# Kernel tuning notes

Hardware: AMD Instinct MI355X
Metric: run time of the kernel (lower is better)

The kernel has to match this reference:

```python
import jax, jax.numpy as jnp
from jax import lax
import numpy as np

B, T, C, V, E, H, OC = 1024, 32, 14, 21128, 200, 50, 8


def gru(x, Wih, Whh, bih, bhh):
    # x: [N, T, E] -> hiddens [N, T, H]; torch nn.GRU gate order (r, z, n)
    Hd = Whh.shape[1]
    xp = jnp.einsum('nte,ge->ntg', x, Wih) + bih  # [N, T, 3H]
    h0 = jnp.zeros((x.shape[0], Hd), x.dtype)

    def step(h, xt):
        gh = h @ Whh.T + bhh
        r = jax.nn.sigmoid(xt[:, :Hd] + gh[:, :Hd])
        z = jax.nn.sigmoid(xt[:, Hd:2 * Hd] + gh[:, Hd:2 * Hd])
        n = jnp.tanh(xt[:, 2 * Hd:] + r * gh[:, 2 * Hd:])
        h_new = (1.0 - z) * n + z * h
        return h_new, h_new

    _, hs = lax.scan(step, h0, jnp.swapaxes(xp, 0, 1))
    return jnp.swapaxes(hs, 0, 1)


def setup_inputs():
    key = jax.random.key(0)
    ks = jax.random.split(key, 32)
    s = 0.1
    inp = {
        'contexts_indices': jax.random.randint(ks[0], (B, T), 0, V),
        'candidates_indices': jax.random.randint(ks[1], (B, C, T), 0, V),
        'y_dev': jax.random.uniform(ks[2], (B, C), dtype=jnp.float32),
        'emb': jax.random.normal(ks[3], (V, E), dtype=jnp.float32),
        'A': jax.random.normal(ks[4], (H, H), dtype=jnp.float32) * s,
        'Wih_c': jax.random.normal(ks[5], (3 * H, E), dtype=jnp.float32) * s,
        'Whh_c': jax.random.normal(ks[6], (3 * H, H), dtype=jnp.float32) * s,
        'bih_c': jnp.zeros((3 * H,), jnp.float32),
        'bhh_c': jnp.zeros((3 * H,), jnp.float32),
        'Wih_r': jax.random.normal(ks[7], (3 * H, E), dtype=jnp.float32) * s,
        'Whh_r': jax.random.normal(ks[8], (3 * H, H), dtype=jnp.float32) * s,
        'bih_r': jnp.zeros((3 * H,), jnp.float32),
        'bhh_r': jnp.zeros((3 * H,), jnp.float32),
        'conv_w': jax.random.normal(ks[9], (OC, 2, 3, 3), dtype=jnp.float32) * s,
        'Wih2': jax.random.normal(ks[10], (3 * H, OC * 10 * 10), dtype=jnp.float32) * s,
        'Whh2': jax.random.normal(ks[11], (3 * H, H), dtype=jnp.float32) * s,
        'bih2': jnp.zeros((3 * H,), jnp.float32),
        'bhh2': jnp.zeros((3 * H,), jnp.float32),
        'fc1_w': jax.random.normal(ks[12], (100, C * H), dtype=jnp.float32) * s,
        'fc1_b': jnp.zeros((100,), jnp.float32),
        'fc2_w': jax.random.normal(ks[13], (C, 100), dtype=jnp.float32) * s,
        'fc2_b': jnp.zeros((C,), jnp.float32),
    }
    return inp


def reference(contexts_indices, candidates_indices, y_dev, emb, A,
              Wih_c, Whh_c, bih_c, bhh_c, Wih_r, Whh_r, bih_r, bhh_r,
              conv_w, Wih2, Whh2, bih2, bhh2, fc1_w, fc1_b, fc2_w, fc2_b):
    b = contexts_indices.shape[0]
    ctx = contexts_indices[:, None, :]                      # [B,1,T]
    ctx_emb = emb[ctx]                                      # [B,1,T,E] (dropout = identity in eval)
    cand_emb = emb[candidates_indices]                      # [B,C,T,E]

    ctx_h = gru(ctx_emb.reshape(-1, T, E), Wih_c, Whh_c, bih_c, bhh_c).reshape(b, 1, T, H)
    cand_h = gru(cand_emb.reshape(-1, T, E), Wih_r, Whh_r, bih_r, bhh_r).reshape(b, C, T, H)

    M1 = jnp.einsum('btph,bcqh->btcpq', ctx_emb, cand_emb)  # [B,1,C,T,T]
    ctx_hA = jnp.einsum('btij,jk->btik', ctx_h, A)
    M2 = jnp.einsum('btph,bcqh->btcpq', ctx_hA, cand_h)

    # faithful to torch: stack on dim 2 then row-major view(-1, 2, T, T)
    M = jnp.stack([M1, M2], axis=2).reshape(-1, 2, T, T)    # [B*C, 2, T, T]

    conv = lax.conv_general_dilated(M, conv_w, (1, 1), 'VALID',
                                    dimension_numbers=('NCHW', 'OIHW', 'NCHW'))  # [B*C, OC, 30, 30]
    pooled = lax.reduce_window(conv, -jnp.inf, lax.max,
                               (1, 1, 3, 3), (1, 1, 3, 3), 'VALID')              # [B*C, OC, 10, 10]

    feats = pooled.reshape(b, C, OC * 10 * 10)              # [B, C, 800]
    Hs = gru(feats, Wih2, Whh2, bih2, bhh2)                 # [B, C, H]
    flat = Hs.reshape(b, -1)                                # [B, C*H]

    hid = jax.nn.relu(flat @ fc1_w.T + fc1_b)
    log_probs = jax.nn.log_softmax(hid @ fc2_w.T + fc2_b, axis=-1)  # softmax then log
    kl = jnp.where(y_dev > 0, y_dev * (jnp.log(y_dev) - log_probs), 0.0)
    return jnp.mean(kl)
```

## Files before the change

kernel.cpp:

```cpp
#include <hip/hip_runtime.h>
#include <math.h>

typedef unsigned short u16;
typedef short s16;
typedef u16 u16x8 __attribute__((ext_vector_type(8)));
typedef s16 short8v __attribute__((ext_vector_type(8)));
typedef float f32x4 __attribute__((ext_vector_type(4)));

__device__ __forceinline__ float b2f(u16 u) {
    return __uint_as_float(((unsigned)u) << 16);
}
__device__ __forceinline__ u16 f2b(float f) {
    unsigned u = __float_as_uint(f);
    unsigned r = (u + 0x7FFFu + ((u >> 16) & 1u)) >> 16;
    return (u16)r;
}

__global__ __launch_bounds__(256) void k_cvt_all(
    const float* __restrict__ emb, u16* __restrict__ embh,
    const float* __restrict__ wcf, u16* __restrict__ wch,
    const float* __restrict__ wrf, u16* __restrict__ wrh,
    const float* __restrict__ w2f, u16* __restrict__ w2h)
{
    long j = (long)blockIdx.x * 256 + threadIdx.x;
    if (j < 1056400) {
        float4 v = ((const float4*)emb)[j];
        *(ushort4*)(embh + j * 4) = make_ushort4(f2b(v.x), f2b(v.y), f2b(v.z), f2b(v.w));
        return;
    }
    j -= 1056400;
    if (j < 7500) {
        float4 v = ((const float4*)wcf)[j];
        *(ushort4*)(wch + j * 4) = make_ushort4(f2b(v.x), f2b(v.y), f2b(v.z), f2b(v.w));
        return;
    }
    j -= 7500;
    if (j < 7500) {
        float4 v = ((const float4*)wrf)[j];
        *(ushort4*)(wrh + j * 4) = make_ushort4(f2b(v.x), f2b(v.y), f2b(v.z), f2b(v.w));
        return;
    }
    j -= 7500;
    if (j < 120000) {
        int jj = (int)(j / 800), k = (int)(j % 800);
        int p = k >> 3, oc = k & 7;
        w2h[jj * 800 + k] = f2b(w2f[jj * 800 + oc * 100 + p]);
    }
}

__global__ __launch_bounds__(256) void k_projmm2(
    const u16* __restrict__ embh, const u16* __restrict__ wc,
    const u16* __restrict__ wr, const float* __restrict__ bc,
    const float* __restrict__ br, u16* __restrict__ outc,
    u16* __restrict__ outr, int V)
{
    __shared__ s16 Ab[2048];
    __shared__ s16 Bb[2560];
    __shared__ float bhL[160];
    const int t = threadIdx.x;
    const int w = t >> 6, l = t & 63, lg = l >> 4, lr = l & 15;
    int id = blockIdx.x;
    const int half = (id >= 662) ? 1 : 0;
    id -= half * 662;
    const u16* wh = half ? wr : wc;
    const float* bias = half ? br : bc;
    u16* outp = half ? outr : outc;
    const int mb = id >> 1, nb = id & 1;
    const long rowbase = (long)mb * 64;
    const int colbase = nb * 80;
    if (t < 160) bhL[t] = (t < 150) ? bias[t] : 0.f;

    f32x4 acc[5];
#pragma unroll
    for (int i = 0; i < 5; ++i) acc[i] = (f32x4){0,0,0,0};

    for (int ch = 0; ch < 7; ++ch) {
        __syncthreads();
        {
            int kc = t >> 6, row = t & 63;
            long grow = rowbase + row; if (grow >= V) grow = V - 1;
            int k0 = ch * 32 + kc * 8;
            short8v v = {0,0,0,0,0,0,0,0};
            if (k0 < 200) v = *(const short8v*)(embh + grow * 200 + k0);
            *(short8v*)&Ab[t * 8] = v;
        }
        for (int it = t; it < 320; it += 256) {
            int kc = it / 80, col = it % 80;
            int gcol = colbase + col;
            int k0 = ch * 32 + kc * 8;
            short8v v = {0,0,0,0,0,0,0,0};
            if (gcol < 150 && k0 < 200)
                v = *(const short8v*)(wh + (size_t)gcol * 200 + k0);
            *(short8v*)&Bb[it * 8] = v;
        }
        __syncthreads();
        short8v a = *(short8v*)&Ab[(lg * 64 + w * 16 + lr) * 8];
#pragma unroll
        for (int ct = 0; ct < 5; ++ct) {
            short8v bv = *(short8v*)&Bb[(lg * 80 + ct * 16 + lr) * 8];
            acc[ct] = __builtin_amdgcn_mfma_f32_16x16x32_bf16(a, bv, acc[ct], 0, 0, 0);
        }
    }
#pragma unroll
    for (int ct = 0; ct < 5; ++ct) {
        int gcol = colbase + ct * 16 + lr;
        if (gcol < 150) {
#pragma unroll
            for (int rr = 0; rr < 4; ++rr) {
                long row = rowbase + w * 16 + lg * 4 + rr;
                outp[row * 152 + gcol] = f2b(acc[ct][rr] + bhL[gcol]);
            }
        }
    }
}

template<int MODE, int SEQS>
__device__ __forceinline__ void gru_body(
    char* sm, const void* __restrict__ xp_, const int* __restrict__ idx,
    const float* __restrict__ Whh, const float* __restrict__ bhh,
    void* __restrict__ hs_, int T, long blk)
{
    s16*   hbuf = (s16*)sm;
    float* ghL  = (float*)(sm + 2048);
    float* hL   = (float*)(sm + 2048 + SEQS * 640);
    float* bhL  = (float*)(sm + 2048 + SEQS * 848);
    u16*   xraw = (u16*)(sm + 2048 + SEQS * 848 + 608);
    const int t = threadIdx.x;
    const int w = t >> 6, l = t & 63, lg = l >> 4, lr = l & 15;
    constexpr int HST = (MODE == 2) ? 56 : 50;
    constexpr int XROW = SEQS * 152;
    u16*   xbH = xraw;
    float* xbF = (float*)xraw;

    for (int li = t; li < 1024; li += 256) hbuf[li] = 0;
    for (int e = t; e < SEQS * 52; e += 256) hL[e] = 0.f;
    if (t < 152) bhL[t] = (t < 150) ? bhh[t] : 0.f;

    const int te_0 = (w * 3     > 9) ? 9 : w * 3;
    const int te_1 = (w * 3 + 1 > 9) ? 9 : w * 3 + 1;
    const int te_2 = (w * 3 + 2 > 9) ? 9 : w * 3 + 2;
    short8v B00 = {0,0,0,0,0,0,0,0}, B01 = B00, B10 = B00, B11 = B00, B20 = B00, B21 = B00;
    {
        int cols[3] = { te_0 * 16 + lr, te_1 * 16 + lr, te_2 * 16 + lr };
        short8v* frg[6] = { &B00, &B01, &B10, &B11, &B20, &B21 };
#pragma unroll
        for (int ti = 0; ti < 3; ++ti) {
            int col = cols[ti];
            if (col < 150) {
#pragma unroll
                for (int s = 0; s < 2; ++s) {
                    short8v v = {0,0,0,0,0,0,0,0};
#pragma unroll
                    for (int e = 0; e < 8; ++e) {
                        int k = (s * 4 + lg) * 8 + e;
                        if (k < 50) v[e] = (s16)f2b(Whh[col * 50 + k]);
                    }
                    *frg[ti * 2 + s] = v;
                }
            }
        }
    }

    const long seqbase = blk * SEQS;
    const float* xpf = (const float*)xp_;
    const u16*   xph = (const u16*)xp_;
    float* hsf = (float*)hs_;
    u16*   hsh = (u16*)hs_;

    const int rA = (MODE == 2) ? t / 19 : t / 38;
    const int oA = (MODE == 2) ? (t % 19) * 8 : (t % 38) * 4;
    const int rB = (MODE == 2) ? (t + 256) / 19 : (t + 256) / 38;
    const int oB = (MODE == 2) ? ((t + 256) % 19) * 8 : ((t + 256) % 38) * 4;
    const bool actA = (MODE == 2) ? (t < SEQS * 19) : true;
    const bool hasB = (MODE == 2) ? (t + 256 < SEQS * 19) : (t + 256 < SEQS * 38);

    auto rowbase = [&](int rr, int stp) -> size_t {
        long r = seqbase + rr;
        long src = (MODE == 0) ? (r * T + stp) : (long)idx[r * T + stp];
        return (size_t)src * 152;
    };

    if (MODE == 2) {
        if (actA) *(u16x8*)&xbH[rA * 152 + oA] = *(const u16x8*)(xph + rowbase(rA, 0) + oA);
        if (hasB) *(u16x8*)&xbH[rB * 152 + oB] = *(const u16x8*)(xph + rowbase(rB, 0) + oB);
    } else {
        *(float4*)&xbF[rA * 152 + oA] = *(const float4*)(xpf + rowbase(rA, 0) + oA);
        if (hasB)
            *(float4*)&xbF[rB * 152 + oB] = *(const float4*)(xpf + rowbase(rB, 0) + oB);
    }
    __syncthreads();

    for (int st = 0; st < T; ++st) {
        const int cur = st & 1;
        u16x8 pfh0, pfh1;
        float4 pf0, pf1;
        if (st + 1 < T) {
            if (MODE == 2) {
                if (actA) pfh0 = *(const u16x8*)(xph + rowbase(rA, st + 1) + oA);
                if (hasB) pfh1 = *(const u16x8*)(xph + rowbase(rB, st + 1) + oB);
            } else {
                pf0 = *(const float4*)(xpf + rowbase(rA, st + 1) + oA);
                if (hasB) pf1 = *(const float4*)(xpf + rowbase(rB, st + 1) + oB);
            }
        }
        short8v a0 = *(short8v*)&hbuf[((0 + lg) * 16 + lr) * 8];
        short8v a1 = *(short8v*)&hbuf[((4 + lg) * 16 + lr) * 8];
        f32x4 c0 = {0,0,0,0}, c1 = {0,0,0,0}, c2 = {0,0,0,0};
        c0 = __builtin_amdgcn_mfma_f32_16x16x32_bf16(a0, B00, c0, 0, 0, 0);
        c0 = __builtin_amdgcn_mfma_f32_16x16x32_bf16(a1, B01, c0, 0, 0, 0);
        c1 = __builtin_amdgcn_mfma_f32_16x16x32_bf16(a0, B10, c1, 0, 0, 0);
        c1 = __builtin_amdgcn_mfma_f32_16x16x32_bf16(a1, B11, c1, 0, 0, 0);
        c2 = __builtin_amdgcn_mfma_f32_16x16x32_bf16(a0, B20, c2, 0, 0, 0);
        c2 = __builtin_amdgcn_mfma_f32_16x16x32_bf16(a1, B21, c2, 0, 0, 0);
        if (lg * 4 < SEQS) {
            int col0 = te_0 * 16 + lr, col1 = te_1 * 16 + lr, col2 = te_2 * 16 + lr;
            if (col0 < 150) {
#pragma unroll
                for (int r = 0; r < 4; ++r) ghL[(lg * 4 + r) * 160 + col0] = c0[r] + bhL[col0];
            }
            if (col1 < 150) {
#pragma unroll
                for (int r = 0; r < 4; ++r) ghL[(lg * 4 + r) * 160 + col1] = c1[r] + bhL[col1];
            }
            if (col2 < 150) {
#pragma unroll
                for (int r = 0; r < 4; ++r) ghL[(lg * 4 + r) * 160 + col2] = c2[r] + bhL[col2];
            }
        }
        __syncthreads();
        if (st + 1 < T) {
            if (MODE == 2) {
                if (actA) *(u16x8*)&xbH[(cur ^ 1) * XROW + rA * 152 + oA] = pfh0;
                if (hasB) *(u16x8*)&xbH[(cur ^ 1) * XROW + rB * 152 + oB] = pfh1;
            } else {
                *(float4*)&xbF[(cur ^ 1) * XROW + rA * 152 + oA] = pf0;
                if (hasB) *(float4*)&xbF[(cur ^ 1) * XROW + rB * 152 + oB] = pf1;
            }
        }
        for (int item = t; item < SEQS * 50; item += 256) {
            int ss = item / 50, hh = item % 50;
            float xv0, xv1, xv2;
            if (MODE == 2) {
                const u16* xr = &xbH[cur * XROW + ss * 152];
                xv0 = b2f(xr[hh]); xv1 = b2f(xr[50 + hh]); xv2 = b2f(xr[100 + hh]);
            } else {
                const float* xr = &xbF[cur * XROW + ss * 152];
                xv0 = xr[hh]; xv1 = xr[50 + hh]; xv2 = xr[100 + hh];
            }
            float vr  = xv0 + ghL[ss * 160 + hh];
            float vz  = xv1 + ghL[ss * 160 + 50 + hh];
            float ghn = ghL[ss * 160 + 100 + hh];
            float rg = 1.f / (1.f + __expf(-vr));
            float zg = 1.f / (1.f + __expf(-vz));
            float a = xv2 + rg * ghn;
            a = fminf(fmaxf(a, -15.f), 15.f);
            float e2 = __expf(-2.f * a);
            float nn2 = (1.f - e2) / (1.f + e2);
            float hn = (1.f - zg) * nn2 + zg * hL[ss * 52 + hh];
            hL[ss * 52 + hh] = hn;
            hbuf[((hh >> 3) * 16 + ss) * 8 + (hh & 7)] = (s16)f2b(hn);
            size_t ofs = ((size_t)(seqbase + ss) * T + st) * HST + hh;
            if (MODE == 2) hsh[ofs] = f2b(hn); else hsf[ofs] = hn;
        }
        __syncthreads();
    }
}

__device__ __forceinline__ void conv_pool_epi(
    char* sm, u16* __restrict__ feats, long nl, f32x4 cacc0, f32x4 cacc1)
{
    s16* pool16 = (s16*)sm;
    float* wL = (float*)(sm + 18960);
    u16* Mb    = (u16*)pool16;
    u16* convL = (u16*)pool16 + 2184;
    const int t = threadIdx.x;
    const int w = t >> 6, l = t & 63, lg = l >> 4, lr = l & 15;
    const int job0 = w * 2, job1 = w * 2 + 1;
    const int ch0 = job0 >> 2, rt0 = (job0 >> 1) & 1, ct0 = job0 & 1;
    const int ch1 = job1 >> 2, rt1 = (job1 >> 1) & 1, ct1 = job1 & 1;

    __syncthreads();
#pragma unroll
    for (int rr = 0; rr < 4; ++rr) {
        Mb[ch0 * 1092 + (rt0 * 16 + lg * 4 + rr) * 33 + ct0 * 16 + lr] = f2b(cacc0[rr]);
        Mb[ch1 * 1092 + (rt1 * 16 + lg * 4 + rr) * 33 + ct1 * 16 + lr] = f2b(cacc1[rr]);
    }

    short8v Bc = {0,0,0,0,0,0,0,0};
    int dlt[8];
#pragma unroll
    for (int e = 0; e < 8; ++e) {
        int s = lg * 8 + e;
        if (s < 18) {
            int ch = s / 9, r9 = s % 9, ky = r9 / 3, kx = r9 % 3;
            dlt[e] = ch * 1092 + ky * 33 + kx;
            if (lr < 8) Bc[e] = (s16)f2b(wL[lr * 18 + s]);
        } else dlt[e] = 0;
    }
    __syncthreads();

    for (int tile = w; tile < 57; tile += 4) {
        int m = tile * 16 + lr;
        int cy = m / 30, cx = m - cy * 30;
        int base = cy * 33 + cx;
        short8v a;
#pragma unroll
        for (int e = 0; e < 8; ++e) a[e] = (s16)Mb[base + dlt[e]];
        f32x4 c = {0,0,0,0};
        c = __builtin_amdgcn_mfma_f32_16x16x32_bf16(a, Bc, c, 0, 0, 0);
        if (lr < 8) {
#pragma unroll
            for (int rr = 0; rr < 4; ++rr)
                convL[(tile * 16 + lg * 4 + rr) * 8 + lr] = f2b(c[rr]);
        }
    }
    __syncthreads();

    if (t < 100) {
        int py = t / 10, px = t % 10;
        int m0 = (3 * py) * 30 + 3 * px;
        float mx[8];
#pragma unroll
        for (int c = 0; c < 8; ++c) mx[c] = -1e30f;
#pragma unroll
        for (int dy = 0; dy < 3; ++dy)
#pragma unroll
            for (int dx = 0; dx < 3; ++dx) {
                u16x8 v = *(u16x8*)&convL[(m0 + dy * 30 + dx) * 8];
#pragma unroll
                for (int c = 0; c < 8; ++c) mx[c] = fmaxf(mx[c], b2f(v[c]));
            }
        u16x8 o;
#pragma unroll
        for (int c = 0; c < 8; ++c) o[c] = f2b(mx[c]);
        *(u16x8*)(feats + nl * 800 + t * 8) = o;
    }
}

__device__ __forceinline__ void m1_body(
    char* sm, const u16* __restrict__ embh, const int* __restrict__ ctx_idx,
    const int* __restrict__ cand_idx, const float* __restrict__ conv_w,
    u16* __restrict__ feats, int wg)
{
    s16* pool16 = (s16*)sm;
    float* wL = (float*)(sm + 18960);
    int* ci = (int*)(sm + 19536);
    int* qi = (int*)(sm + 19664);
    const int t = threadIdx.x;
    const int xcd = wg & 7, q = wg >> 3;
    const int r = q % 7, bq = q / 7;
    const int b = bq * 8 + xcd;
    const long nl = (long)b * 14 + r;
    const int w = t >> 6, l = t & 63, lg = l >> 4, lr = l & 15;

    if (t < 144) wL[t] = conv_w[t];

    f32x4 cacc0 = {0,0,0,0}, cacc1 = {0,0,0,0};
    const int job0 = w * 2, job1 = w * 2 + 1;
    const int ch0 = job0 >> 2, rt0 = (job0 >> 1) & 1, ct0 = job0 & 1;
    const int ch1 = job1 >> 2, rt1 = (job1 >> 1) & 1, ct1 = job1 & 1;

    const int c0 = 2 * r;
    if (t < 32) ci[t] = ctx_idx[b * 32 + t];
    else if (t < 96)
        qi[((t - 32) >> 5) * 32 + (t & 31)] =
            cand_idx[((long)b * 14 + c0 + ((t - 32) >> 5)) * 32 + (t & 31)];
    __syncthreads();
    s16* ctxL = pool16;
    s16* canL = pool16 + 3168;
#pragma unroll
    for (int cnk = 0; cnk < 3; ++cnk) {
        const int kcbase = (cnk == 0) ? 0 : (cnk == 1 ? 12 : 20);
        const int kccnt  = (cnk == 0) ? 12 : 8;
        const int scnt   = (cnk == 0) ? 3 : 2;
        if (cnk) __syncthreads();
        for (int it = t; it < kccnt * 32; it += 256) {
            int kcl = it >> 5, row = it & 31;
            int kc = kcbase + kcl;
            short8v v = {0,0,0,0,0,0,0,0};
            if (kc < 25) v = *(const short8v*)(embh + (size_t)ci[row] * 200 + kc * 8);
            *(short8v*)&ctxL[(kcl * 33 + row) * 8] = v;
        }
        for (int it = t; it < kccnt * 64; it += 256) {
            int kcl = it >> 6, col = it & 63;
            int kc = kcbase + kcl;
            short8v v = {0,0,0,0,0,0,0,0};
            if (kc < 25)
                v = *(const short8v*)(embh + (size_t)qi[(col >> 5) * 32 + (col & 31)] * 200 + kc * 8);
            *(short8v*)&canL[(kcl * 65 + col) * 8] = v;
        }
        __syncthreads();
        for (int sl = 0; sl < scnt; ++sl) {
            int kcl = sl * 4 + lg;
            short8v a0 = *(short8v*)&ctxL[(kcl * 33 + rt0 * 16 + lr) * 8];
            short8v b0 = *(short8v*)&canL[(kcl * 65 + ch0 * 32 + ct0 * 16 + lr) * 8];
            short8v b1 = *(short8v*)&canL[(kcl * 65 + ch1 * 32 + ct1 * 16 + lr) * 8];
            cacc0 = __builtin_amdgcn_mfma_f32_16x16x32_bf16(a0, b0, cacc0, 0, 0, 0);
            short8v a1 = (rt0 == rt1) ? a0
                       : *(short8v*)&ctxL[(kcl * 33 + rt1 * 16 + lr) * 8];
            cacc1 = __builtin_amdgcn_mfma_f32_16x16x32_bf16(a1, b1, cacc1, 0, 0, 0);
        }
    }
    conv_pool_epi(sm, feats, nl, cacc0, cacc1);
}

__global__ __launch_bounds__(256) void k_scan_m1(
    const u16* __restrict__ proj_ch, const u16* __restrict__ proj_rh,
    const int* __restrict__ ctx_idx, const int* __restrict__ cand_idx,
    const float* __restrict__ Whh_c, const float* __restrict__ Whh_r,
    const float* __restrict__ bhh_c, const float* __restrict__ bhh_r,
    u16* __restrict__ ctx_hh, u16* __restrict__ candh_h,
    const u16* __restrict__ embh, const float* __restrict__ conv_w,
    u16* __restrict__ feats)
{
    __shared__ long long smq[3244];
    char* sm = (char*)smq;
    const long bid = blockIdx.x;
    if (bid < 960) {
        const bool cand = (bid < 896);
        gru_body<2, 16>(sm,
                        cand ? (const void*)proj_rh : (const void*)proj_ch,
                        cand ? cand_idx : ctx_idx,
                        cand ? Whh_r : Whh_c,
                        cand ? bhh_r : bhh_c,
                        cand ? (void*)candh_h : (void*)ctx_hh,
                        32, cand ? bid : bid - 896);
    } else {
        m1_body(sm, embh, ctx_idx, cand_idx, conv_w, feats, (int)(bid - 960));
    }
}

__global__ __launch_bounds__(256) void k_m2conv(
    const u16* __restrict__ ctxA_h, const u16* __restrict__ candh_h,
    const float* __restrict__ conv_w, u16* __restrict__ feats)
{
    __shared__ long long smq[2490];
    char* sm = (char*)smq;
    s16* pool16 = (s16*)sm;
    float* wL = (float*)(sm + 18960);
    const int t = threadIdx.x;
    const int wg = blockIdx.x;
    const int xcd = wg & 7, q = wg >> 3;
    const int r7 = q % 7, bq = q / 7;
    const int b = bq * 8 + xcd;
    const long nl = (long)b * 14 + 7 + r7;
    const int w = t >> 6, l = t & 63, lg = l >> 4, lr = l & 15;

    if (t < 144) wL[t] = conv_w[t];

    f32x4 cacc0 = {0,0,0,0}, cacc1 = {0,0,0,0};
    const int job0 = w * 2, job1 = w * 2 + 1;
    const int ch0 = job0 >> 2, rt0 = (job0 >> 1) & 1, ct0 = job0 & 1;
    const int ch1 = job1 >> 2, rt1 = (job1 >> 1) & 1, ct1 = job1 & 1;

    const int c0 = 2 * r7;
    s16* aL = pool16;
    s16* cL = pool16 + 2112;
    for (int it = t; it < 256; it += 256) {
        int kc = it >> 5, row = it & 31;
        short8v v = {0,0,0,0,0,0,0,0};
        if (kc < 7) {
            v = *(const short8v*)(ctxA_h + (size_t)(b * 32 + row) * 56 + kc * 8);
            if (kc == 6) { v[2] = 0; v[3] = 0; v[4] = 0; v[5] = 0; v[6] = 0; v[7] = 0; }
        }
        *(short8v*)&aL[(kc * 33 + row) * 8] = v;
    }
    for (int it = t; it < 512; it += 256) {
        int kc = it >> 6, col = it & 63;
        long row = ((long)b * 14 + c0 + (col >> 5)) * 32 + (col & 31);
        short8v v = {0,0,0,0,0,0,0,0};
        if (kc < 7) {
            v = *(const short8v*)(candh_h + (size_t)row * 56 + kc * 8);
            if (kc == 6) { v[2] = 0; v[3] = 0; v[4] = 0; v[5] = 0; v[6] = 0; v[7] = 0; }
        }
        *(short8v*)&cL[(kc * 65 + col) * 8] = v;
    }
    __syncthreads();
#pragma unroll
    for (int sl = 0; sl < 2; ++sl) {
        int kcl = sl * 4 + lg;
        short8v a0 = *(short8v*)&aL[(kcl * 33 + rt0 * 16 + lr) * 8];
        short8v b0 = *(short8v*)&cL[(kcl * 65 + ch0 * 32 + ct0 * 16 + lr) * 8];
        short8v b1 = *(short8v*)&cL[(kcl * 65 + ch1 * 32 + ct1 * 16 + lr) * 8];
        cacc0 = __builtin_amdgcn_mfma_f32_16x16x32_bf16(a0, b0, cacc0, 0, 0, 0);
        short8v a1 = (rt0 == rt1) ? a0
                   : *(short8v*)&aL[(kcl * 33 + rt1 * 16 + lr) * 8];
        cacc1 = __builtin_amdgcn_mfma_f32_16x16x32_bf16(a1, b1, cacc1, 0, 0, 0);
    }
    conv_pool_epi(sm, feats, nl, cacc0, cacc1);
}

__global__ __launch_bounds__(256) void k_scan2(
    const float* __restrict__ xp2, const float* __restrict__ Whh2,
    const float* __restrict__ bhh2, float* __restrict__ hs2)
{
    __shared__ long long smq[2396];
    gru_body<0, 8>((char*)smq, xp2, nullptr, Whh2, bhh2, hs2, 14, (long)blockIdx.x);
}

__global__ __launch_bounds__(256) void k_matA(
    const u16* __restrict__ inh, const float* __restrict__ A,
    u16* __restrict__ outh)
{
    __shared__ float AL[50 * 52];
    __shared__ float inL[32 * 52];
    const int t = threadIdx.x;
    for (int e = t; e < 2500; e += 256) AL[(e / 50) * 52 + (e % 50)] = A[e];
    const long rbase = (long)blockIdx.x * 32;
    for (int e = t; e < 1600; e += 256) {
        int r = e / 50, j = e % 50;
        inL[r * 52 + j] = b2f(inh[(rbase + r) * 56 + j]);
    }
    __syncthreads();
    for (int item = t; item < 1600; item += 256) {
        int r = item / 50, kk = item % 50;
        float acc = 0.f;
#pragma unroll 10
        for (int j = 0; j < 50; ++j)
            acc += inL[r * 52 + j] * AL[j * 52 + kk];
        outh[(rbase + r) * 56 + kk] = f2b(acc);
    }
}

__global__ __launch_bounds__(256) void k_xp2mm(
    const u16* __restrict__ feats, const u16* __restrict__ w2h,
    const float* __restrict__ bih2, float* __restrict__ out)
{
    __shared__ s16 Ab[2048];
    __shared__ s16 Bb[2560];
    __shared__ float bhL[160];
    const int t = threadIdx.x;
    const int w = t >> 6, l = t & 63, lg = l >> 4, lr = l & 15;
    const int mb = blockIdx.x >> 1, nb = blockIdx.x & 1;
    const long rowbase = (long)mb * 64;
    const int colbase = nb * 80;
    if (t < 160) bhL[t] = (t < 150) ? bih2[t] : 0.f;

    f32x4 acc[5];
#pragma unroll
    for (int i = 0; i < 5; ++i) acc[i] = (f32x4){0,0,0,0};

    for (int ch = 0; ch < 25; ++ch) {
        __syncthreads();
        {
            int kc = t >> 6, row = t & 63;
            *(short8v*)&Ab[t * 8] =
                *(const short8v*)(feats + (rowbase + row) * 800 + ch * 32 + kc * 8);
        }
        for (int it = t; it < 320; it += 256) {
            int kc = it / 80, col = it % 80;
            int gcol = colbase + col;
            short8v v = {0,0,0,0,0,0,0,0};
            if (gcol < 150)
                v = *(const short8v*)(w2h + (size_t)gcol * 800 + ch * 32 + kc * 8);
            *(short8v*)&Bb[it * 8] = v;
        }
        __syncthreads();
        short8v a = *(short8v*)&Ab[(lg * 64 + w * 16 + lr) * 8];
#pragma unroll
        for (int ct = 0; ct < 5; ++ct) {
            short8v bv = *(short8v*)&Bb[(lg * 80 + ct * 16 + lr) * 8];
            acc[ct] = __builtin_amdgcn_mfma_f32_16x16x32_bf16(a, bv, acc[ct], 0, 0, 0);
        }
    }
#pragma unroll
    for (int ct = 0; ct < 5; ++ct) {
        int gcol = colbase + ct * 16 + lr;
        if (gcol < 150) {
#pragma unroll
            for (int rr = 0; rr < 4; ++rr) {
                long row = rowbase + w * 16 + lg * 4 + rr;
                out[row * 152 + gcol] = acc[ct][rr] + bhL[gcol];
            }
        }
    }
}

__global__ __launch_bounds__(128) void k_head(
    const float* __restrict__ Hs, const float* __restrict__ w1,
    const float* __restrict__ b1, const float* __restrict__ w2,
    const float* __restrict__ b2, const float* __restrict__ y,
    float* __restrict__ partial)
{
    __shared__ float hr[700];
    __shared__ float hidL[100];
    const int t = threadIdx.x;
    const long b = blockIdx.x;
    for (int e = t; e < 700; e += 128) hr[e] = Hs[b * 700 + e];
    __syncthreads();
    if (t < 100) {
        float acc = b1[t];
        const float4* wp = (const float4*)(w1 + (size_t)t * 700);
        for (int k4 = 0; k4 < 175; ++k4) {
            float4 wv = wp[k4];
            float4 hv = *(float4*)&hr[k4 * 4];
            acc += wv.x * hv.x + wv.y * hv.y + wv.z * hv.z + wv.w * hv.w;
        }
        hidL[t] = fmaxf(acc, 0.f);
    }
    __syncthreads();
    if (t < 64) {
        float logit = -1e30f;
        if (t < 14) {
            logit = b2[t];
            for (int k = 0; k < 100; ++k) logit += hidL[k] * w2[t * 100 + k];
        }
        float m = logit;
        for (int off = 8; off; off >>= 1) m = fmaxf(m, __shfl_xor(m, off, 16));
        float ex = (t < 14) ? __expf(logit - m) : 0.f;
        float se = ex;
        for (int off = 8; off; off >>= 1) se += __shfl_xor(se, off, 16);
        float kl = 0.f;
        if (t < 14) {
            float lp = logit - m - __logf(se);
            float yv = y[b * 14 + t];
            kl = (yv > 0.f) ? yv * (__logf(yv) - lp) : 0.f;
        }
        for (int off = 8; off; off >>= 1) kl += __shfl_xor(kl, off, 16);
        if (t == 0) partial[b] = kl;
    }
}

__global__ __launch_bounds__(256) void k_reduce(
    const float* __restrict__ partial, float* __restrict__ out)
{
    __shared__ float sm[256];
    const int t = threadIdx.x;
    sm[t] = partial[t] + partial[t + 256] + partial[t + 512] + partial[t + 768];
    __syncthreads();
    for (int off = 128; off; off >>= 1) {
        if (t < off) sm[t] += sm[t + off];
        __syncthreads();
    }
    if (t == 0) out[0] = sm[0] * (1.f / 14336.f);
}

extern "C" void kernel_launch(void* const* d_in, const int* in_sizes, int n_in,
                              void* d_out, int out_size, void* d_ws, size_t ws_size,
                              hipStream_t stream)
{
    const int*   ctx_idx  = (const int*)d_in[0];
    const int*   cand_idx = (const int*)d_in[1];
    const float* y_dev    = (const float*)d_in[2];
    const float* emb      = (const float*)d_in[3];
    const float* A        = (const float*)d_in[4];
    const float* Wih_c    = (const float*)d_in[5];
    const float* Whh_c    = (const float*)d_in[6];
    const float* bih_c    = (const float*)d_in[7];
    const float* bhh_c    = (const float*)d_in[8];
    const float* Wih_r    = (const float*)d_in[9];
    const float* Whh_r    = (const float*)d_in[10];
    const float* bih_r    = (const float*)d_in[11];
    const float* bhh_r    = (const float*)d_in[12];
    const float* conv_w   = (const float*)d_in[13];
    const float* Wih2     = (const float*)d_in[14];
    const float* Whh2     = (const float*)d_in[15];
    const float* bih2     = (const float*)d_in[16];
    const float* bhh2     = (const float*)d_in[17];
    const float* fc1_w    = (const float*)d_in[18];
    const float* fc1_b    = (const float*)d_in[19];
    const float* fc2_w    = (const float*)d_in[20];
    const float* fc2_b    = (const float*)d_in[21];

    float* ws = (float*)d_ws;
    u16*   embh    = (u16*)ws;
    u16*   proj_ch = (u16*)(ws + 2112800);
    u16*   proj_rh = (u16*)(ws + 3722784);
    u16*   ctx_hh  = (u16*)(ws + 5332768);
    u16*   ctxA_h  = (u16*)(ws + 6250272);
    u16*   candh_h = (u16*)(ws + 7167776);
    u16*   feats_h = (u16*)(ws + 20012832);
    u16*   w2h     = (u16*)(ws + 25747232);
    u16*   wch     = (u16*)(ws + 25807232);
    u16*   wrh     = (u16*)(ws + 25822232);
    float* xp2     = ws + 25837232;
    float* hs2     = ws + 28016304;
    float* part    = ws + 28733104;

    k_cvt_all <<<4654, 256, 0, stream>>>(emb, embh, Wih_c, wch, Wih_r, wrh,
                                         Wih2, w2h);
    k_projmm2 <<<1324, 256, 0, stream>>>(embh, wch, wrh, bih_c, bih_r,
                                         proj_ch, proj_rh, 21128);
    k_scan_m1 <<<8128, 256, 0, stream>>>(proj_ch, proj_rh, ctx_idx, cand_idx,
                                         Whh_c, Whh_r, bhh_c, bhh_r,
                                         ctx_hh, candh_h, embh, conv_w, feats_h);
    k_matA <<<1024, 256, 0, stream>>>(ctx_hh, A, ctxA_h);
    k_m2conv <<<7168, 256, 0, stream>>>(ctxA_h, candh_h, conv_w, feats_h);
    k_xp2mm <<<448, 256, 0, stream>>>(feats_h, w2h, bih2, xp2);
    k_scan2 <<<128, 256, 0, stream>>>(xp2, Whh2, bhh2, hs2);
    k_head <<<1024, 128, 0, stream>>>(hs2, fc1_w, fc1_b, fc2_w, fc2_b, y_dev, part);
    k_reduce <<<1, 256, 0, stream>>>(part, (float*)d_out);
}
```

Measured before the change: 303.9 us.

## Loop seven candidate pairs per M1 block, reusing context embeddings in LDS

The M1 conv path now launches one workgroup per batch row instead of one per (batch, candidate-pair). Each workgroup loads the full 200-wide context embedding into LDS once and loops over the 7 candidate pairs, so the redundant context gathers disappear. The conv/pool epilogue is split into two half-passes so its LDS scratch fits in a smaller buffer, and k_m2conv's shared memory shrinks to match. The trade-off is far fewer blocks in the M1 portion and serialised work per block, which may reduce parallelism and latency hiding.

After: 317.0 us. 1.04x slower.

```diff
diff --git a/kernel.cpp b/kernel.cpp
--- a/kernel.cpp
+++ b/kernel.cpp
@@ -266,13 +266,12 @@
     }
 }
 
-__device__ __forceinline__ void conv_pool_epi(
-    char* sm, u16* __restrict__ feats, long nl, f32x4 cacc0, f32x4 cacc1)
-{
-    s16* pool16 = (s16*)sm;
-    float* wL = (float*)(sm + 18960);
-    u16* Mb    = (u16*)pool16;
-    u16* convL = (u16*)pool16 + 2184;
+__device__ __forceinline__ void conv_pool_epi2(
+    s16* pool, short8v Bc, const int* dlt,
+    u16* __restrict__ feats, long nl, f32x4 cacc0, f32x4 cacc1)
+{
+    u16* Mb    = (u16*)pool;
+    u16* convL = (u16*)pool + 2184;
     const int t = threadIdx.x;
     const int w = t >> 6, l = t & 63, lg = l >> 4, lr = l & 15;
     const int job0 = w * 2, job1 = w * 2 + 1;
@@ -285,7 +284,106 @@
         Mb[ch0 * 1092 + (rt0 * 16 + lg * 4 + rr) * 33 + ct0 * 16 + lr] = f2b(cacc0[rr]);
         Mb[ch1 * 1092 + (rt1 * 16 + lg * 4 + rr) * 33 + ct1 * 16 + lr] = f2b(cacc1[rr]);
     }
-
+    __syncthreads();
+
+    for (int tile = w; tile < 29; tile += 4) {
+        int m = tile * 16 + lr;
+        int cy = m / 30, cx = m - cy * 30;
+        int base = cy * 33 + cx;
+        short8v a;
+#pragma unroll
+        for (int e = 0; e < 8; ++e) a[e] = (s16)Mb[base + dlt[e]];
+        f32x4 c = {0,0,0,0};
+        c = __builtin_amdgcn_mfma_f32_16x16x32_bf16(a, Bc, c, 0, 0, 0);
+        if (lr < 8) {
+#pragma unroll
+            for (int rr = 0; rr < 4; ++rr)
+                convL[(tile * 16 + lg * 4 + rr) * 8 + lr] = f2b(c[rr]);
+        }
+    }
+    __syncthreads();
+    if (t < 50) {
+        int py = t / 10, px = t % 10;
+        int m0 = (3 * py) * 30 + 3 * px;
+        float mx[8];
+#pragma unroll
+        for (int c = 0; c < 8; ++c) mx[c] = -1e30f;
+#pragma unroll
+        for (int dy = 0; dy < 3; ++dy)
+#pragma unroll
+            for (int dx = 0; dx < 3; ++dx) {
+                u16x8 v = *(u16x8*)&convL[(m0 + dy * 30 + dx) * 8];
+#pragma unroll
+                for (int c = 0; c < 8; ++c) mx[c] = fmaxf(mx[c], b2f(v[c]));
+            }
+        u16x8 o;
+#pragma unroll
+        for (int c = 0; c < 8; ++c) o[c] = f2b(mx[c]);
+        *(u16x8*)(feats + nl * 800 + t * 8) = o;
+    }
+    __syncthreads();
+    for (int tile = 28 + w; tile < 57; tile += 4) {
+        int m = tile * 16 + lr;
+        int cy = m / 30, cx = m - cy * 30;
+        int base = cy * 33 + cx;
+        short8v a;
+#pragma unroll
+        for (int e = 0; e < 8; ++e) a[e] = (s16)Mb[base + dlt[e]];
+        f32x4 c = {0,0,0,0};
+        c = __builtin_amdgcn_mfma_f32_16x16x32_bf16(a, Bc, c, 0, 0, 0);
+        if (lr < 8) {
+#pragma unroll
+            for (int rr = 0; rr < 4; ++rr)
+                convL[(tile * 16 + lg * 4 + rr - 448) * 8 + lr] = f2b(c[rr]);
+        }
+    }
+    __syncthreads();
+    if (t < 50) {
+        int py = 5 + t / 10, px = t % 10;
+        int m0 = (3 * py) * 30 + 3 * px - 448;
+        float mx[8];
+#pragma unroll
+        for (int c = 0; c < 8; ++c) mx[c] = -1e30f;
+#pragma unroll
+        for (int dy = 0; dy < 3; ++dy)
+#pragma unroll
+            for (int dx = 0; dx < 3; ++dx) {
+                u16x8 v = *(u16x8*)&convL[(m0 + dy * 30 + dx) * 8];
+#pragma unroll
+                for (int c = 0; c < 8; ++c) mx[c] = fmaxf(mx[c], b2f(v[c]));
+            }
+        u16x8 o;
+#pragma unroll
+        for (int c = 0; c < 8; ++c) o[c] = f2b(mx[c]);
+        *(u16x8*)(feats + nl * 800 + (50 + t) * 8) = o;
+    }
+    __syncthreads();
+}
+
+__device__ __forceinline__ void m1_super(
+    char* sm, const u16* __restrict__ embh, const int* __restrict__ ctx_idx,
+    const int* __restrict__ cand_idx, const float* __restrict__ conv_w,
+    u16* __restrict__ feats, int m)
+{
+    s16* ctxL = (s16*)sm;
+    s16* canL = (s16*)sm + 6600;
+    float* wL = (float*)(sm + 25680);
+    int* ci = (int*)(sm + 26256);
+    int* qi = (int*)(sm + 26384);
+    const int t = threadIdx.x;
+    const int xcd = m & 7, bq = m >> 3;
+    const int b = bq * 8 + xcd;
+    const int w = t >> 6, l = t & 63, lg = l >> 4, lr = l & 15;
+
+    if (t < 144) wL[t] = conv_w[t];
+    if (t >= 160 && t < 192) ci[t - 160] = ctx_idx[b * 32 + (t - 160)];
+    __syncthreads();
+
+    for (int it = t; it < 800; it += 256) {
+        int kc = it >> 5, row = it & 31;
+        *(short8v*)&ctxL[(kc * 33 + row) * 8] =
+            *(const short8v*)(embh + (size_t)ci[row] * 200 + kc * 8);
+    }
     short8v Bc = {0,0,0,0,0,0,0,0};
     int dlt[8];
 #pragma unroll
@@ -297,111 +395,44 @@
             if (lr < 8) Bc[e] = (s16)f2b(wL[lr * 18 + s]);
         } else dlt[e] = 0;
     }
-    __syncthreads();
-
-    for (int tile = w; tile < 57; tile += 4) {
-        int m = tile * 16 + lr;
-        int cy = m / 30, cx = m - cy * 30;
-        int base = cy * 33 + cx;
-        short8v a;
-#pragma unroll
-        for (int e = 0; e < 8; ++e) a[e] = (s16)Mb[base + dlt[e]];
-        f32x4 c = {0,0,0,0};
-        c = __builtin_amdgcn_mfma_f32_16x16x32_bf16(a, Bc, c, 0, 0, 0);
-        if (lr < 8) {
-#pragma unroll
-            for (int rr = 0; rr < 4; ++rr)
-                convL[(tile * 16 + lg * 4 + rr) * 8 + lr] = f2b(c[rr]);
-        }
-    }
-    __syncthreads();
-
-    if (t < 100) {
-        int py = t / 10, px = t % 10;
-        int m0 = (3 * py) * 30 + 3 * px;
-        float mx[8];
-#pragma unroll
-        for (int c = 0; c < 8; ++c) mx[c] = -1e30f;
-#pragma unroll
-        for (int dy = 0; dy < 3; ++dy)
-#pragma unroll
-            for (int dx = 0; dx < 3; ++dx) {
-                u16x8 v = *(u16x8*)&convL[(m0 + dy * 30 + dx) * 8];
-#pragma unroll
-                for (int c = 0; c < 8; ++c) mx[c] = fmaxf(mx[c], b2f(v[c]));
-            }
-        u16x8 o;
-#pragma unroll
-        for (int c = 0; c < 8; ++c) o[c] = f2b(mx[c]);
-        *(u16x8*)(feats + nl * 800 + t * 8) = o;
-    }
-}
-
-__device__ __forceinline__ void m1_body(
-    char* sm, const u16* __restrict__ embh, const int* __restrict__ ctx_idx,
-    const int* __restrict__ cand_idx, const float* __restrict__ conv_w,
-    u16* __restrict__ feats, int wg)
-{
-    s16* pool16 = (s16*)sm;
-    float* wL = (float*)(sm + 18960);
-    int* ci = (int*)(sm + 19536);
-    int* qi = (int*)(sm + 19664);
-    const int t = threadIdx.x;
-    const int xcd = wg & 7, q = wg >> 3;
-    const int r = q % 7, bq = q / 7;
-    const int b = bq * 8 + xcd;
-    const long nl = (long)b * 14 + r;
-    const int w = t >> 6, l = t & 63, lg = l >> 4, lr = l & 15;
-
-    if (t < 144) wL[t] = conv_w[t];
-
-    f32x4 cacc0 = {0,0,0,0}, cacc1 = {0,0,0,0};
+
     const int job0 = w * 2, job1 = w * 2 + 1;
     const int ch0 = job0 >> 2, rt0 = (job0 >> 1) & 1, ct0 = job0 & 1;
     const int ch1 = job1 >> 2, rt1 = (job1 >> 1) & 1, ct1 = job1 & 1;
 
-    const int c0 = 2 * r;
-    if (t < 32) ci[t] = ctx_idx[b * 32 + t];
-    else if (t < 96)
-        qi[((t - 32) >> 5) * 32 + (t & 31)] =
-            cand_idx[((long)b * 14 + c0 + ((t - 32) >> 5)) * 32 + (t & 31)];
-    __syncthreads();
-    s16* ctxL = pool16;
-    s16* canL = pool16 + 3168;
-#pragma unroll
-    for (int cnk = 0; cnk < 3; ++cnk) {
-        const int kcbase = (cnk == 0) ? 0 : (cnk == 1 ? 12 : 20);
-        const int kccnt  = (cnk == 0) ? 12 : 8;
-        const int scnt   = (cnk == 0) ? 3 : 2;
-        if (cnk) __syncthreads();
-        for (int it = t; it < kccnt * 32; it += 256) {
-            int kcl = it >> 5, row = it & 31;
-            int kc = kcbase + kcl;
-            short8v v = {0,0,0,0,0,0,0,0};
-            if (kc < 25) v = *(const short8v*)(embh + (size_t)ci[row] * 200 + kc * 8);
-            *(short8v*)&ctxL[(kcl * 33 + row) * 8] = v;
-        }
-        for (int it = t; it < kccnt * 64; it += 256) {
-            int kcl = it >> 6, col = it & 63;
-            int kc = kcbase + kcl;
-            short8v v = {0,0,0,0,0,0,0,0};
-            if (kc < 25)
-                v = *(const short8v*)(embh + (size_t)qi[(col >> 5) * 32 + (col & 31)] * 200 + kc * 8);
-            *(short8v*)&canL[(kcl * 65 + col) * 8] = v;
-        }
-        __syncthreads();
-        for (int sl = 0; sl < scnt; ++sl) {
-            int kcl = sl * 4 + lg;
-            short8v a0 = *(short8v*)&ctxL[(kcl * 33 + rt0 * 16 + lr) * 8];
-            short8v b0 = *(short8v*)&canL[(kcl * 65 + ch0 * 32 + ct0 * 16 + lr) * 8];
-            short8v b1 = *(short8v*)&canL[(kcl * 65 + ch1 * 32 + ct1 * 16 + lr) * 8];
-            cacc0 = __builtin_amdgcn_mfma_f32_16x16x32_bf16(a0, b0, cacc0, 0, 0, 0);
-            short8v a1 = (rt0 == rt1) ? a0
-                       : *(short8v*)&ctxL[(kcl * 33 + rt1 * 16 + lr) * 8];
-            cacc1 = __builtin_amdgcn_mfma_f32_16x16x32_bf16(a1, b1, cacc1, 0, 0, 0);
-        }
-    }
-    conv_pool_epi(sm, feats, nl, cacc0, cacc1);
+    for (int r = 0; r < 7; ++r) {
+        if (t < 64)
+            qi[t] = cand_idx[((long)b * 14 + 2 * r + (t >> 5)) * 32 + (t & 31)];
+        f32x4 cacc0 = {0,0,0,0}, cacc1 = {0,0,0,0};
+#pragma unroll
+        for (int cnk = 0; cnk < 3; ++cnk) {
+            const int kcbase = (cnk == 0) ? 0 : (cnk == 1 ? 12 : 20);
+            const int kccnt  = (cnk == 0) ? 12 : 8;
+            const int scnt   = (cnk == 0) ? 3 : 2;
+            __syncthreads();
+            for (int it = t; it < kccnt * 64; it += 256) {
+                int kcl = it >> 6, col = it & 63;
+                int kc = kcbase + kcl;
+                short8v v = {0,0,0,0,0,0,0,0};
+                if (kc < 25)
+                    v = *(const short8v*)(embh + (size_t)qi[(col >> 5) * 32 + (col & 31)] * 200 + kc * 8);
+                *(short8v*)&canL[(kcl * 65 + col) * 8] = v;
+            }
+            __syncthreads();
+            for (int sl = 0; sl < scnt; ++sl) {
+                int kcl = sl * 4 + lg;
+                int kc = kcbase + kcl;
+                short8v a0 = *(short8v*)&ctxL[(kc * 33 + rt0 * 16 + lr) * 8];
+                short8v b0 = *(short8v*)&canL[(kcl * 65 + ch0 * 32 + ct0 * 16 + lr) * 8];
+                short8v b1 = *(short8v*)&canL[(kcl * 65 + ch1 * 32 + ct1 * 16 + lr) * 8];
+                cacc0 = __builtin_amdgcn_mfma_f32_16x16x32_bf16(a0, b0, cacc0, 0, 0, 0);
+                short8v a1 = (rt0 == rt1) ? a0
+                           : *(short8v*)&ctxL[(kc * 33 + rt1 * 16 + lr) * 8];
+                cacc1 = __builtin_amdgcn_mfma_f32_16x16x32_bf16(a1, b1, cacc1, 0, 0, 0);
+            }
+        }
+        conv_pool_epi2(canL, Bc, dlt, feats, (long)b * 14 + r, cacc0, cacc1);
+    }
 }
 
 __global__ __launch_bounds__(256) void k_scan_m1(
@@ -413,7 +444,7 @@
     const u16* __restrict__ embh, const float* __restrict__ conv_w,
     u16* __restrict__ feats)
 {
-    __shared__ long long smq[3244];
+    __shared__ long long smq[3330];
     char* sm = (char*)smq;
     const long bid = blockIdx.x;
     if (bid < 960) {
@@ -426,7 +457,7 @@
                         cand ? (void*)candh_h : (void*)ctx_hh,
                         32, cand ? bid : bid - 896);
     } else {
-        m1_body(sm, embh, ctx_idx, cand_idx, conv_w, feats, (int)(bid - 960));
+        m1_super(sm, embh, ctx_idx, cand_idx, conv_w, feats, (int)(bid - 960));
     }
 }
 
@@ -434,10 +465,11 @@
     const u16* __restrict__ ctxA_h, const u16* __restrict__ candh_h,
     const float* __restrict__ conv_w, u16* __restrict__ feats)
 {
-    __shared__ long long smq[2490];
+    __shared__ long long smq[1640];
     char* sm = (char*)smq;
-    s16* pool16 = (s16*)sm;
-    float* wL = (float*)(sm + 18960);
+    s16* aL = (s16*)sm;
+    s16* cL = (s16*)sm + 2112;
+    float* wL = (float*)(sm + 12544);
     const int t = threadIdx.x;
     const int wg = blockIdx.x;
     const int xcd = wg & 7, q = wg >> 3;
@@ -454,8 +486,6 @@
     const int ch1 = job1 >> 2, rt1 = (job1 >> 1) & 1, ct1 = job1 & 1;
 
     const int c0 = 2 * r7;
-    s16* aL = pool16;
-    s16* cL = pool16 + 2112;
     for (int it = t; it < 256; it += 256) {
         int kc = it >> 5, row = it & 31;
         short8v v = {0,0,0,0,0,0,0,0};
@@ -476,6 +506,19 @@
         *(short8v*)&cL[(kc * 65 + col) * 8] = v;
     }
     __syncthreads();
+
+    short8v Bc = {0,0,0,0,0,0,0,0};
+    int dlt[8];
+#pragma unroll
+    for (int e = 0; e < 8; ++e) {
+        int s = lg * 8 + e;
+        if (s < 18) {
+            int ch = s / 9, r9 = s % 9, ky = r9 / 3, kx = r9 % 3;
+            dlt[e] = ch * 1092 + ky * 33 + kx;
+            if (lr < 8) Bc[e] = (s16)f2b(wL[lr * 18 + s]);
+        } else dlt[e] = 0;
+    }
+
 #pragma unroll
     for (int sl = 0; sl < 2; ++sl) {
         int kcl = sl * 4 + lg;
@@ -487,7 +530,7 @@
                    : *(short8v*)&aL[(kcl * 33 + rt1 * 16 + lr) * 8];
         cacc1 = __builtin_amdgcn_mfma_f32_16x16x32_bf16(a1, b1, cacc1, 0, 0, 0);
     }
-    conv_pool_epi(sm, feats, nl, cacc0, cacc1);
+    conv_pool_epi2((s16*)sm, Bc, dlt, feats, nl, cacc0, cacc1);
 }
 
 __global__ __launch_bounds__(256) void k_scan2(
@@ -681,7 +724,7 @@
                                          Wih2, w2h);
     k_projmm2 <<<1324, 256, 0, stream>>>(embh, wch, wrh, bih_c, bih_r,
                                          proj_ch, proj_rh, 21128);
-    k_scan_m1 <<<8128, 256, 0, stream>>>(proj_ch, proj_rh, ctx_idx, cand_idx,
+    k_scan_m1 <<<1984, 256, 0, stream>>>(proj_ch, proj_rh, ctx_idx, cand_idx,
                                          Whh_c, Whh_r, bhh_c, bhh_r,
                                          ctx_hh, candh_h, embh, conv_w, feats_h);
     k_matA <<<1024, 256, 0, stream>>>(ctx_hh, A, ctxA_h);
```
